# Kernel optimization log

Hardware: AMD Instinct MI355X
Metric: run time of the kernel (lower is better)

## Reference

```python
import jax, jax.numpy as jnp
import numpy as np

B, H, NQ, NL, NA = 262144, 256, 4, 2, 16


def _apply_1q(s, U, q):
    # s: [B, 2,2,2,2]; U: [B,2,2] (batched) or [2,2] (shared)
    s = jnp.moveaxis(s, 1 + q, -1)
    if U.ndim == 3:
        s = jnp.einsum('bij,b...j->b...i', U, s)
    else:
        s = jnp.einsum('ij,b...j->b...i', U, s)
    return jnp.moveaxis(s, -1, 1 + q)


def _apply_cnot(s, c, t):
    s = jnp.moveaxis(s, (1 + c, 1 + t), (-2, -1))
    s = jnp.stack([s[..., 0, :], s[..., 1, ::-1]], axis=-2)  # flip target when control=1
    return jnp.moveaxis(s, (-2, -1), (1 + c, 1 + t))


def _rx(theta):
    # batched RX: theta [B] -> [B,2,2]
    c = jnp.cos(theta / 2).astype(jnp.complex64)
    s = (-1j) * jnp.sin(theta / 2)
    return jnp.stack([jnp.stack([c, s], -1), jnp.stack([s, c], -1)], -2)


def _rot(phi, theta, omega):
    # PennyLane Rot = RZ(omega) @ RY(theta) @ RZ(phi), scalar angles -> [2,2]
    c, s = jnp.cos(theta / 2), jnp.sin(theta / 2)
    return jnp.array(1, jnp.complex64) * jnp.stack([
        jnp.stack([jnp.exp(-0.5j * (phi + omega)) * c, -jnp.exp(0.5j * (phi - omega)) * s], -1),
        jnp.stack([jnp.exp(-0.5j * (phi - omega)) * s, jnp.exp(0.5j * (phi + omega)) * c], -1),
    ], -2)


def _circuit(angles, q_weights):
    # angles: [B, NQ] -> PauliZ expvals [B, NQ] via 4-qubit state-vector sim
    b = angles.shape[0]
    s = jnp.zeros((b,) + (2,) * NQ, jnp.complex64)
    s = s.at[(slice(None),) + (0,) * NQ].set(1.0)
    for q in range(NQ):  # AngleEmbedding (RX rotations)
        s = _apply_1q(s, _rx(angles[:, q]), q)
    for l in range(NL):  # StronglyEntanglingLayers
        for w in range(NQ):
            s = _apply_1q(s, _rot(q_weights[l, w, 0], q_weights[l, w, 1], q_weights[l, w, 2]), w)
        r = l % (NQ - 1) + 1
        for w in range(NQ):
            s = _apply_cnot(s, w, (w + r) % NQ)
    probs = s.real ** 2 + s.imag ** 2  # [B,2,2,2,2]
    zs = []
    axes = tuple(range(1, NQ + 1))
    for q in range(NQ):
        p = probs.sum(tuple(a for a in axes if a != 1 + q))  # [B,2]
        zs.append(p[:, 0] - p[:, 1])
    return jnp.stack(zs, axis=1)


def setup_inputs() -> dict:
    key = jax.random.key(0)
    ks = jax.random.split(key, 6)
    return {
        'h': jax.random.normal(ks[0], (B, H), jnp.float32),
        'W_embed': jax.random.normal(ks[1], (NQ, H), jnp.float32) / np.sqrt(H),
        'b_embed': jnp.zeros((NQ,), jnp.float32),
        'q_weights': jax.random.uniform(ks[2], (NL, NQ, 3), jnp.float32, 0.0, 2 * np.pi),
        'W_out': jax.random.normal(ks[3], (NA, NQ), jnp.float32) / np.sqrt(NQ),
        'b_out': jnp.zeros((NA,), jnp.float32),
    }


def reference(h, W_embed, b_embed, q_weights, W_out, b_out):
    angles = jnp.tanh(h @ W_embed.T + b_embed)  # [B, NQ]
    z = _circuit(angles, q_weights)             # [B, NQ]
    return z @ W_out.T + b_out                  # [B, NA]
```

## Files before the change

kernel.cpp:

```cpp
#include <hip/hip_runtime.h>

#define NQ 4
#define NL 2
#define NA 16
#define HDIM 256
#define BLK 64
#define RPB 64

template<int M>
__device__ __forceinline__ void apply_u(float* sr, float* si, const float* u) {
    const float u00r = u[0], u00i = u[1], u01r = u[2], u01i = u[3];
    const float u10r = u[4], u10i = u[5], u11r = u[6], u11i = u[7];
#pragma unroll
    for (int k = 0; k < 16; ++k) {
        if (k & M) continue;
        const int k1 = k | M;
        const float a0r = sr[k],  a0i = si[k];
        const float a1r = sr[k1], a1i = si[k1];
        sr[k]  = u00r*a0r - u00i*a0i + u01r*a1r - u01i*a1i;
        si[k]  = u00r*a0i + u00i*a0r + u01r*a1i + u01i*a1r;
        sr[k1] = u10r*a0r - u10i*a0i + u11r*a1r - u11i*a1i;
        si[k1] = u10r*a0i + u10i*a0r + u11r*a1i + u11i*a1r;
    }
}

template<int MC, int MT>
__device__ __forceinline__ void cnot(float* sr, float* si) {
#pragma unroll
    for (int k = 0; k < 16; ++k) {
        if ((k & MC) && !(k & MT)) {
            const int k1 = k | MT;
            float tr = sr[k]; sr[k] = sr[k1]; sr[k1] = tr;
            float ti = si[k]; si[k] = si[k1]; si[k1] = ti;
        }
    }
}

__global__ __launch_bounds__(BLK) void qph_kernel(
    const float* __restrict__ h,
    const float* __restrict__ W_embed,
    const float* __restrict__ b_embed,
    const float* __restrict__ q_weights,
    const float* __restrict__ W_out,
    const float* __restrict__ b_out,
    float* __restrict__ out,
    int B)
{
    __shared__ __align__(16) float w_lds[NQ * HDIM];
    __shared__ float rot_lds[NL * NQ][8];
    __shared__ float wout_lds[NA * NQ];
    __shared__ float bout_lds[NA];

    const int tid = threadIdx.x;
    const long rowBase = (long)blockIdx.x * RPB;

#pragma unroll
    for (int k = 0; k < 16; ++k) w_lds[tid + k * BLK] = W_embed[tid + k * BLK];
    if (tid < NA * NQ) wout_lds[tid] = W_out[tid];
    if (tid < NA)      bout_lds[tid] = b_out[tid];
    if (tid < NL * NQ) {
        const float phi = q_weights[tid * 3 + 0];
        const float th  = q_weights[tid * 3 + 1];
        const float om  = q_weights[tid * 3 + 2];
        const float c  = cosf(0.5f * th), s  = sinf(0.5f * th);
        const float al = 0.5f * (phi + om), be = 0.5f * (phi - om);
        const float ca = cosf(al), sa = sinf(al);
        const float cb = cosf(be), sb = sinf(be);
        rot_lds[tid][0] =  ca * c;  rot_lds[tid][1] = -sa * c;
        rot_lds[tid][2] = -cb * s;  rot_lds[tid][3] = -sb * s;
        rot_lds[tid][4] =  cb * s;  rot_lds[tid][5] = -sb * s;
        rot_lds[tid][6] =  ca * c;  rot_lds[tid][7] =  sa * c;
    }
    __syncthreads();

    const int t = tid & 3;
    const int g = tid >> 2;
    const float be0 = b_embed[0], be1 = b_embed[1], be2 = b_embed[2], be3 = b_embed[3];

    float my0 = 0.f, my1 = 0.f, my2 = 0.f, my3 = 0.f;

#pragma unroll
    for (int rr = 0; rr < 4; ++rr) {
        const int  lrow = g * 4 + rr;
        const long grow = rowBase + lrow;
        float acc0 = 0.f, acc1 = 0.f, acc2 = 0.f, acc3 = 0.f;
        if (grow < B) {
            const float4* hrow = (const float4*)(h + grow * (long)HDIM);
#pragma unroll
            for (int j = 0; j < 16; ++j) {
                const float4 hv = hrow[j * 4 + t];
                const float4 w0 = *(const float4*)&w_lds[0 * HDIM + j * 16 + t * 4];
                const float4 w1 = *(const float4*)&w_lds[1 * HDIM + j * 16 + t * 4];
                const float4 w2 = *(const float4*)&w_lds[2 * HDIM + j * 16 + t * 4];
                const float4 w3 = *(const float4*)&w_lds[3 * HDIM + j * 16 + t * 4];
                acc0 = fmaf(hv.x, w0.x, fmaf(hv.y, w0.y, fmaf(hv.z, w0.z, fmaf(hv.w, w0.w, acc0))));
                acc1 = fmaf(hv.x, w1.x, fmaf(hv.y, w1.y, fmaf(hv.z, w1.z, fmaf(hv.w, w1.w, acc1))));
                acc2 = fmaf(hv.x, w2.x, fmaf(hv.y, w2.y, fmaf(hv.z, w2.z, fmaf(hv.w, w2.w, acc2))));
                acc3 = fmaf(hv.x, w3.x, fmaf(hv.y, w3.y, fmaf(hv.z, w3.z, fmaf(hv.w, w3.w, acc3))));
            }
        }
        acc0 += __shfl_xor(acc0, 1); acc0 += __shfl_xor(acc0, 2);
        acc1 += __shfl_xor(acc1, 1); acc1 += __shfl_xor(acc1, 2);
        acc2 += __shfl_xor(acc2, 1); acc2 += __shfl_xor(acc2, 2);
        acc3 += __shfl_xor(acc3, 1); acc3 += __shfl_xor(acc3, 2);
        if (t == rr) { my0 = acc0; my1 = acc1; my2 = acc2; my3 = acc3; }
    }

    const long grow = rowBase + tid;
    if (grow >= B) return;

    const float angs[4] = {tanhf(my0 + be0), tanhf(my1 + be1),
                           tanhf(my2 + be2), tanhf(my3 + be3)};

    float sr[16], si[16];
#pragma unroll
    for (int k = 0; k < 16; ++k) { sr[k] = 0.f; si[k] = 0.f; }
    sr[0] = 1.0f;

#pragma unroll
    for (int q = 0; q < NQ; ++q) {
        const float th = angs[q];
        const float c = __cosf(0.5f * th), s = __sinf(0.5f * th);
        const int m = 8 >> q;
#pragma unroll
        for (int k = 0; k < 16; ++k) {
            if (k & m) continue;
            const int k1 = k | m;
            const float a0r = sr[k],  a0i = si[k];
            const float a1r = sr[k1], a1i = si[k1];
            sr[k]  = c * a0r + s * a1i;
            si[k]  = c * a0i - s * a1r;
            sr[k1] = s * a0i + c * a1r;
            si[k1] = c * a1i - s * a0r;
        }
    }

    apply_u<8>(sr, si, rot_lds[0]);
    apply_u<4>(sr, si, rot_lds[1]);
    apply_u<2>(sr, si, rot_lds[2]);
    apply_u<1>(sr, si, rot_lds[3]);
    cnot<8, 4>(sr, si);
    cnot<4, 2>(sr, si);
    cnot<2, 1>(sr, si);
    cnot<1, 8>(sr, si);
    apply_u<8>(sr, si, rot_lds[4]);
    apply_u<4>(sr, si, rot_lds[5]);
    apply_u<2>(sr, si, rot_lds[6]);
    apply_u<1>(sr, si, rot_lds[7]);
    cnot<8, 2>(sr, si);
    cnot<4, 1>(sr, si);
    cnot<2, 8>(sr, si);
    cnot<1, 4>(sr, si);

    float p[16];
#pragma unroll
    for (int k = 0; k < 16; ++k) p[k] = sr[k] * sr[k] + si[k] * si[k];
    float z[4];
#pragma unroll
    for (int q = 0; q < NQ; ++q) {
        const int m = 8 >> q;
        float zz = 0.f;
#pragma unroll
        for (int k = 0; k < 16; ++k) zz += (k & m) ? -p[k] : p[k];
        z[q] = zz;
    }

    float4* out4 = (float4*)(out + grow * (long)NA);
#pragma unroll
    for (int i = 0; i < 4; ++i) {
        float o[4];
#pragma unroll
        for (int jj = 0; jj < 4; ++jj) {
            const int a = i * 4 + jj;
            float v = bout_lds[a];
#pragma unroll
            for (int q = 0; q < NQ; ++q) v = fmaf(z[q], wout_lds[a * 4 + q], v);
            o[jj] = v;
        }
        out4[i] = make_float4(o[0], o[1], o[2], o[3]);
    }
}

extern "C" void kernel_launch(void* const* d_in, const int* in_sizes, int n_in,
                              void* d_out, int out_size, void* d_ws, size_t ws_size,
                              hipStream_t stream) {
    const float* h         = (const float*)d_in[0];
    const float* W_embed   = (const float*)d_in[1];
    const float* b_embed   = (const float*)d_in[2];
    const float* q_weights = (const float*)d_in[3];
    const float* W_out     = (const float*)d_in[4];
    const float* b_out     = (const float*)d_in[5];
    float* out = (float*)d_out;

    const int B = in_sizes[0] / HDIM;
    const int blocks = (B + RPB - 1) / RPB;
    qph_kernel<<<blocks, BLK, 0, stream>>>(h, W_embed, b_embed, q_weights, W_out, b_out, out, B);
}
```

Before: 57.77 us.

## Double-buffer h rows into LDS via async global_load_lds with register-held weights

Raises the block to 256 threads and 256 rows, and streams h in 16-row tiles into a double-buffered LDS region using async global-to-LDS loads, overlapping the next tile's load with the current tile's dot products. W_embed now lives in registers per lane instead of LDS. The 16-lane shuffle reduction assigns each row's embedding to one thread, and z values are staged through LDS so each thread writes one output row. This adds register pressure and relies on hand-placed waitcnt values being correct. Each wave waits only on its own loads and there is no barrier between tiles, so reading rows loaded by other waves may be racy.

```diff
diff --git a/kernel.cpp b/kernel.cpp
--- a/kernel.cpp
+++ b/kernel.cpp
@@ -4,8 +4,16 @@
 #define NL 2
 #define NA 16
 #define HDIM 256
-#define BLK 64
-#define RPB 64
+#define BLK 256
+#define RPB 256
+#define TROWS 16
+#define NTILES (RPB / TROWS)
+
+__device__ __forceinline__ void gload_lds16(const float* g, float* l) {
+    __builtin_amdgcn_global_load_lds(
+        (const __attribute__((address_space(1))) void*)g,
+        (__attribute__((address_space(3))) void*)l, 16, 0, 0);
+}
 
 template<int M>
 __device__ __forceinline__ void apply_u(float* sr, float* si, const float* u) {
@@ -46,136 +54,164 @@
     float* __restrict__ out,
     int B)
 {
-    __shared__ __align__(16) float w_lds[NQ * HDIM];
+    __shared__ __align__(16) float hbuf[2][TROWS * HDIM];
     __shared__ float rot_lds[NL * NQ][8];
     __shared__ float wout_lds[NA * NQ];
     __shared__ float bout_lds[NA];
-
-    const int tid = threadIdx.x;
+    __shared__ __align__(16) float zbuf[RPB][4];
+
+    const int tid  = threadIdx.x;
+    const int lane = tid & 63;
+    const int w    = tid >> 6;
+    const int c    = lane & 15;
+    const int rit  = tid >> 4;
     const long rowBase = (long)blockIdx.x * RPB;
 
-#pragma unroll
-    for (int k = 0; k < 16; ++k) w_lds[tid + k * BLK] = W_embed[tid + k * BLK];
     if (tid < NA * NQ) wout_lds[tid] = W_out[tid];
     if (tid < NA)      bout_lds[tid] = b_out[tid];
     if (tid < NL * NQ) {
         const float phi = q_weights[tid * 3 + 0];
         const float th  = q_weights[tid * 3 + 1];
         const float om  = q_weights[tid * 3 + 2];
-        const float c  = cosf(0.5f * th), s  = sinf(0.5f * th);
+        const float cc = cosf(0.5f * th), ss = sinf(0.5f * th);
         const float al = 0.5f * (phi + om), be = 0.5f * (phi - om);
         const float ca = cosf(al), sa = sinf(al);
         const float cb = cosf(be), sb = sinf(be);
-        rot_lds[tid][0] =  ca * c;  rot_lds[tid][1] = -sa * c;
-        rot_lds[tid][2] = -cb * s;  rot_lds[tid][3] = -sb * s;
-        rot_lds[tid][4] =  cb * s;  rot_lds[tid][5] = -sb * s;
-        rot_lds[tid][6] =  ca * c;  rot_lds[tid][7] =  sa * c;
+        rot_lds[tid][0] =  ca * cc;  rot_lds[tid][1] = -sa * cc;
+        rot_lds[tid][2] = -cb * ss;  rot_lds[tid][3] = -sb * ss;
+        rot_lds[tid][4] =  cb * ss;  rot_lds[tid][5] = -sb * ss;
+        rot_lds[tid][6] =  ca * cc;  rot_lds[tid][7] =  sa * cc;
     }
     __syncthreads();
 
-    const int t = tid & 3;
-    const int g = tid >> 2;
+    float4 wreg[NQ][4];
+#pragma unroll
+    for (int q = 0; q < NQ; ++q)
+#pragma unroll
+        for (int j = 0; j < 4; ++j)
+            wreg[q][j] = *(const float4*)(W_embed + q * HDIM + c * 4 + j * 64);
     const float be0 = b_embed[0], be1 = b_embed[1], be2 = b_embed[2], be3 = b_embed[3];
 
+#define ISSUE_TILE(T, b)                                                        \
+    {                                                                           \
+        _Pragma("unroll")                                                       \
+        for (int r = 0; r < 4; ++r) {                                           \
+            long srow = rowBase + (long)(T) * TROWS + w * 4 + r;                \
+            if (srow > (long)B - 1) srow = (long)B - 1;                         \
+            gload_lds16(h + srow * HDIM + lane * 4,                             \
+                        &hbuf[b][(w * 4 + r) * HDIM]);                          \
+        }                                                                       \
+    }
+
+    ISSUE_TILE(0, 0);
+
     float my0 = 0.f, my1 = 0.f, my2 = 0.f, my3 = 0.f;
 
 #pragma unroll
-    for (int rr = 0; rr < 4; ++rr) {
-        const int  lrow = g * 4 + rr;
-        const long grow = rowBase + lrow;
-        float acc0 = 0.f, acc1 = 0.f, acc2 = 0.f, acc3 = 0.f;
-        if (grow < B) {
-            const float4* hrow = (const float4*)(h + grow * (long)HDIM);
-#pragma unroll
-            for (int j = 0; j < 16; ++j) {
-                const float4 hv = hrow[j * 4 + t];
-                const float4 w0 = *(const float4*)&w_lds[0 * HDIM + j * 16 + t * 4];
-                const float4 w1 = *(const float4*)&w_lds[1 * HDIM + j * 16 + t * 4];
-                const float4 w2 = *(const float4*)&w_lds[2 * HDIM + j * 16 + t * 4];
-                const float4 w3 = *(const float4*)&w_lds[3 * HDIM + j * 16 + t * 4];
-                acc0 = fmaf(hv.x, w0.x, fmaf(hv.y, w0.y, fmaf(hv.z, w0.z, fmaf(hv.w, w0.w, acc0))));
-                acc1 = fmaf(hv.x, w1.x, fmaf(hv.y, w1.y, fmaf(hv.z, w1.z, fmaf(hv.w, w1.w, acc1))));
-                acc2 = fmaf(hv.x, w2.x, fmaf(hv.y, w2.y, fmaf(hv.z, w2.z, fmaf(hv.w, w2.w, acc2))));
-                acc3 = fmaf(hv.x, w3.x, fmaf(hv.y, w3.y, fmaf(hv.z, w3.z, fmaf(hv.w, w3.w, acc3))));
+    for (int T = 0; T < NTILES; ++T) {
+        if (T + 1 < NTILES) {
+            ISSUE_TILE(T + 1, (T + 1) & 1);
+            asm volatile("s_waitcnt vmcnt(4)" ::: "memory");
+        } else {
+            asm volatile("s_waitcnt vmcnt(0)" ::: "memory");
+        }
+        __builtin_amdgcn_sched_barrier(0);
+
+        const float* hb = &hbuf[T & 1][rit * HDIM];
+        float a0 = 0.f, a1 = 0.f, a2 = 0.f, a3 = 0.f;
+#pragma unroll
+        for (int j = 0; j < 4; ++j) {
+            const float4 hv = *(const float4*)&hb[c * 4 + j * 64];
+            const float4 w0 = wreg[0][j], w1 = wreg[1][j], w2 = wreg[2][j], w3 = wreg[3][j];
+            a0 = fmaf(hv.x, w0.x, fmaf(hv.y, w0.y, fmaf(hv.z, w0.z, fmaf(hv.w, w0.w, a0))));
+            a1 = fmaf(hv.x, w1.x, fmaf(hv.y, w1.y, fmaf(hv.z, w1.z, fmaf(hv.w, w1.w, a1))));
+            a2 = fmaf(hv.x, w2.x, fmaf(hv.y, w2.y, fmaf(hv.z, w2.z, fmaf(hv.w, w2.w, a2))));
+            a3 = fmaf(hv.x, w3.x, fmaf(hv.y, w3.y, fmaf(hv.z, w3.z, fmaf(hv.w, w3.w, a3))));
+        }
+        a0 += __shfl_xor(a0, 1); a0 += __shfl_xor(a0, 2); a0 += __shfl_xor(a0, 4); a0 += __shfl_xor(a0, 8);
+        a1 += __shfl_xor(a1, 1); a1 += __shfl_xor(a1, 2); a1 += __shfl_xor(a1, 4); a1 += __shfl_xor(a1, 8);
+        a2 += __shfl_xor(a2, 1); a2 += __shfl_xor(a2, 2); a2 += __shfl_xor(a2, 4); a2 += __shfl_xor(a2, 8);
+        a3 += __shfl_xor(a3, 1); a3 += __shfl_xor(a3, 2); a3 += __shfl_xor(a3, 4); a3 += __shfl_xor(a3, 8);
+        if (c == T) { my0 = a0; my1 = a1; my2 = a2; my3 = a3; }
+    }
+#undef ISSUE_TILE
+
+    const int  lrow = c * 16 + rit;
+    const long grow = rowBase + lrow;
+
+    if (grow < B) {
+        const float angs[4] = {tanhf(my0 + be0), tanhf(my1 + be1),
+                               tanhf(my2 + be2), tanhf(my3 + be3)};
+
+        float sr[16], si[16];
+#pragma unroll
+        for (int k = 0; k < 16; ++k) { sr[k] = 0.f; si[k] = 0.f; }
+        sr[0] = 1.0f;
+
+#pragma unroll
+        for (int q = 0; q < NQ; ++q) {
+            const float th = angs[q];
+            const float cc = __cosf(0.5f * th), ss = __sinf(0.5f * th);
+            const int m = 8 >> q;
+#pragma unroll
+            for (int k = 0; k < 16; ++k) {
+                if (k & m) continue;
+                const int k1 = k | m;
+                const float r0 = sr[k],  i0 = si[k];
+                const float r1 = sr[k1], i1 = si[k1];
+                sr[k]  = cc * r0 + ss * i1;
+                si[k]  = cc * i0 - ss * r1;
+                sr[k1] = ss * i0 + cc * r1;
+                si[k1] = cc * i1 - ss * r0;
             }
         }
-        acc0 += __shfl_xor(acc0, 1); acc0 += __shfl_xor(acc0, 2);
-        acc1 += __shfl_xor(acc1, 1); acc1 += __shfl_xor(acc1, 2);
-        acc2 += __shfl_xor(acc2, 1); acc2 += __shfl_xor(acc2, 2);
-        acc3 += __shfl_xor(acc3, 1); acc3 += __shfl_xor(acc3, 2);
-        if (t == rr) { my0 = acc0; my1 = acc1; my2 = acc2; my3 = acc3; }
-    }
-
-    const long grow = rowBase + tid;
-    if (grow >= B) return;
-
-    const float angs[4] = {tanhf(my0 + be0), tanhf(my1 + be1),
-                           tanhf(my2 + be2), tanhf(my3 + be3)};
-
-    float sr[16], si[16];
-#pragma unroll
-    for (int k = 0; k < 16; ++k) { sr[k] = 0.f; si[k] = 0.f; }
-    sr[0] = 1.0f;
-
-#pragma unroll
-    for (int q = 0; q < NQ; ++q) {
-        const float th = angs[q];
-        const float c = __cosf(0.5f * th), s = __sinf(0.5f * th);
-        const int m = 8 >> q;
-#pragma unroll
-        for (int k = 0; k < 16; ++k) {
-            if (k & m) continue;
-            const int k1 = k | m;
-            const float a0r = sr[k],  a0i = si[k];
-            const float a1r = sr[k1], a1i = si[k1];
-            sr[k]  = c * a0r + s * a1i;
-            si[k]  = c * a0i - s * a1r;
-            sr[k1] = s * a0i + c * a1r;
-            si[k1] = c * a1i - s * a0r;
-        }
-    }
-
-    apply_u<8>(sr, si, rot_lds[0]);
-    apply_u<4>(sr, si, rot_lds[1]);
-    apply_u<2>(sr, si, rot_lds[2]);
-    apply_u<1>(sr, si, rot_lds[3]);
-    cnot<8, 4>(sr, si);
-    cnot<4, 2>(sr, si);
-    cnot<2, 1>(sr, si);
-    cnot<1, 8>(sr, si);
-    apply_u<8>(sr, si, rot_lds[4]);
-    apply_u<4>(sr, si, rot_lds[5]);
-    apply_u<2>(sr, si, rot_lds[6]);
-    apply_u<1>(sr, si, rot_lds[7]);
-    cnot<8, 2>(sr, si);
-    cnot<4, 1>(sr, si);
-    cnot<2, 8>(sr, si);
-    cnot<1, 4>(sr, si);
-
-    float p[16];
-#pragma unroll
-    for (int k = 0; k < 16; ++k) p[k] = sr[k] * sr[k] + si[k] * si[k];
-    float z[4];
-#pragma unroll
-    for (int q = 0; q < NQ; ++q) {
-        const int m = 8 >> q;
-        float zz = 0.f;
-#pragma unroll
-        for (int k = 0; k < 16; ++k) zz += (k & m) ? -p[k] : p[k];
-        z[q] = zz;
-    }
-
-    float4* out4 = (float4*)(out + grow * (long)NA);
+
+        apply_u<8>(sr, si, rot_lds[0]);
+        apply_u<4>(sr, si, rot_lds[1]);
+        apply_u<2>(sr, si, rot_lds[2]);
+        apply_u<1>(sr, si, rot_lds[3]);
+        cnot<8, 4>(sr, si);
+        cnot<4, 2>(sr, si);
+        cnot<2, 1>(sr, si);
+        cnot<1, 8>(sr, si);
+        apply_u<8>(sr, si, rot_lds[4]);
+        apply_u<4>(sr, si, rot_lds[5]);
+        apply_u<2>(sr, si, rot_lds[6]);
+        apply_u<1>(sr, si, rot_lds[7]);
+        cnot<8, 2>(sr, si);
+        cnot<4, 1>(sr, si);
+        cnot<2, 8>(sr, si);
+        cnot<1, 4>(sr, si);
+
+        float p[16];
+#pragma unroll
+        for (int k = 0; k < 16; ++k) p[k] = sr[k] * sr[k] + si[k] * si[k];
+        float zt[4];
+#pragma unroll
+        for (int q = 0; q < NQ; ++q) {
+            const int m = 8 >> q;
+            float zz = 0.f;
+#pragma unroll
+            for (int k = 0; k < 16; ++k) zz += (k & m) ? -p[k] : p[k];
+            zt[q] = zz;
+        }
+        *(float4*)&zbuf[lrow][0] = make_float4(zt[0], zt[1], zt[2], zt[3]);
+    }
+    __syncthreads();
+
+    const long orow = rowBase + tid;
+    if (orow >= B) return;
+    const float4 zv = *(const float4*)&zbuf[tid][0];
+
+    float4* out4 = (float4*)(out + orow * (long)NA);
 #pragma unroll
     for (int i = 0; i < 4; ++i) {
         float o[4];
 #pragma unroll
         for (int jj = 0; jj < 4; ++jj) {
             const int a = i * 4 + jj;
-            float v = bout_lds[a];
-#pragma unroll
-            for (int q = 0; q < NQ; ++q) v = fmaf(z[q], wout_lds[a * 4 + q], v);
-            o[jj] = v;
+            const float4 wv = *(const float4*)&wout_lds[a * 4];
+            o[jj] = bout_lds[a] + zv.x * wv.x + zv.y * wv.y + zv.z * wv.z + zv.w * wv.w;
         }
         out4[i] = make_float4(o[0], o[1], o[2], o[3]);
     }
```

New measurement: 62.42 us. +8.0%, slower.

## Stream h rows wave-wide with register-resident W_embed and butterfly reduction

Applied to the files above, without the earlier changes.

Restructures the embedding matvec so that each of the 64 lanes holds one float4 slice of every W_embed row in registers. The block then iterates over its 64 rows with fully coalesced 1 KB row loads, and the four per-row dot products are combined with a transposed shuffle butterfly. Results are redistributed to one row per thread through a small LDS buffer. This removes the LDS traffic for W_embed and gives contiguous global loads, at the cost of many more cross-lane shuffles per row and a fully unrolled 64-iteration loop.

```diff
diff --git a/kernel.cpp b/kernel.cpp
--- a/kernel.cpp
+++ b/kernel.cpp
@@ -6,6 +6,10 @@
 #define HDIM 256
 #define BLK 64
 #define RPB 64
+
+__device__ __forceinline__ float dot4(float4 a, float4 b) {
+    return fmaf(a.x, b.x, fmaf(a.y, b.y, fmaf(a.z, b.z, a.w * b.w)));
+}
 
 template<int M>
 __device__ __forceinline__ void apply_u(float* sr, float* si, const float* u) {
@@ -46,71 +50,84 @@
     float* __restrict__ out,
     int B)
 {
-    __shared__ __align__(16) float w_lds[NQ * HDIM];
     __shared__ float rot_lds[NL * NQ][8];
     __shared__ float wout_lds[NA * NQ];
     __shared__ float bout_lds[NA];
-
-    const int tid = threadIdx.x;
+    __shared__ __align__(16) float tbuf[RPB * 4];
+
+    const int l = threadIdx.x;
+    const int t = l & 3;
+    const int g = l >> 2;
     const long rowBase = (long)blockIdx.x * RPB;
 
-#pragma unroll
-    for (int k = 0; k < 16; ++k) w_lds[tid + k * BLK] = W_embed[tid + k * BLK];
-    if (tid < NA * NQ) wout_lds[tid] = W_out[tid];
-    if (tid < NA)      bout_lds[tid] = b_out[tid];
-    if (tid < NL * NQ) {
-        const float phi = q_weights[tid * 3 + 0];
-        const float th  = q_weights[tid * 3 + 1];
-        const float om  = q_weights[tid * 3 + 2];
+    if (l < NA * NQ) wout_lds[l] = W_out[l];
+    if (l < NA)      bout_lds[l] = b_out[l];
+    if (l < NL * NQ) {
+        const float phi = q_weights[l * 3 + 0];
+        const float th  = q_weights[l * 3 + 1];
+        const float om  = q_weights[l * 3 + 2];
         const float c  = cosf(0.5f * th), s  = sinf(0.5f * th);
         const float al = 0.5f * (phi + om), be = 0.5f * (phi - om);
         const float ca = cosf(al), sa = sinf(al);
         const float cb = cosf(be), sb = sinf(be);
-        rot_lds[tid][0] =  ca * c;  rot_lds[tid][1] = -sa * c;
-        rot_lds[tid][2] = -cb * s;  rot_lds[tid][3] = -sb * s;
-        rot_lds[tid][4] =  cb * s;  rot_lds[tid][5] = -sb * s;
-        rot_lds[tid][6] =  ca * c;  rot_lds[tid][7] =  sa * c;
-    }
+        rot_lds[l][0] =  ca * c;  rot_lds[l][1] = -sa * c;
+        rot_lds[l][2] = -cb * s;  rot_lds[l][3] = -sb * s;
+        rot_lds[l][4] =  cb * s;  rot_lds[l][5] = -sb * s;
+        rot_lds[l][6] =  ca * c;  rot_lds[l][7] =  sa * c;
+    }
+
+    float4 wq0 = *(const float4*)(W_embed + 0 * HDIM + 4 * l);
+    float4 wq1 = *(const float4*)(W_embed + 1 * HDIM + 4 * l);
+    float4 wq2 = *(const float4*)(W_embed + 2 * HDIM + 4 * l);
+    float4 wq3 = *(const float4*)(W_embed + 3 * HDIM + 4 * l);
     __syncthreads();
 
-    const int t = tid & 3;
-    const int g = tid >> 2;
-    const float be0 = b_embed[0], be1 = b_embed[1], be2 = b_embed[2], be3 = b_embed[3];
-
-    float my0 = 0.f, my1 = 0.f, my2 = 0.f, my3 = 0.f;
-
-#pragma unroll
-    for (int rr = 0; rr < 4; ++rr) {
-        const int  lrow = g * 4 + rr;
-        const long grow = rowBase + lrow;
-        float acc0 = 0.f, acc1 = 0.f, acc2 = 0.f, acc3 = 0.f;
-        if (grow < B) {
-            const float4* hrow = (const float4*)(h + grow * (long)HDIM);
-#pragma unroll
-            for (int j = 0; j < 16; ++j) {
-                const float4 hv = hrow[j * 4 + t];
-                const float4 w0 = *(const float4*)&w_lds[0 * HDIM + j * 16 + t * 4];
-                const float4 w1 = *(const float4*)&w_lds[1 * HDIM + j * 16 + t * 4];
-                const float4 w2 = *(const float4*)&w_lds[2 * HDIM + j * 16 + t * 4];
-                const float4 w3 = *(const float4*)&w_lds[3 * HDIM + j * 16 + t * 4];
-                acc0 = fmaf(hv.x, w0.x, fmaf(hv.y, w0.y, fmaf(hv.z, w0.z, fmaf(hv.w, w0.w, acc0))));
-                acc1 = fmaf(hv.x, w1.x, fmaf(hv.y, w1.y, fmaf(hv.z, w1.z, fmaf(hv.w, w1.w, acc1))));
-                acc2 = fmaf(hv.x, w2.x, fmaf(hv.y, w2.y, fmaf(hv.z, w2.z, fmaf(hv.w, w2.w, acc2))));
-                acc3 = fmaf(hv.x, w3.x, fmaf(hv.y, w3.y, fmaf(hv.z, w3.z, fmaf(hv.w, w3.w, acc3))));
-            }
-        }
-        acc0 += __shfl_xor(acc0, 1); acc0 += __shfl_xor(acc0, 2);
-        acc1 += __shfl_xor(acc1, 1); acc1 += __shfl_xor(acc1, 2);
-        acc2 += __shfl_xor(acc2, 1); acc2 += __shfl_xor(acc2, 2);
-        acc3 += __shfl_xor(acc3, 1); acc3 += __shfl_xor(acc3, 2);
-        if (t == rr) { my0 = acc0; my1 = acc1; my2 = acc2; my3 = acc3; }
-    }
-
-    const long grow = rowBase + tid;
+    float keep0 = 0.f, keep1 = 0.f, keep2 = 0.f, keep3 = 0.f;
+    const float4* __restrict__ h4 = (const float4*)h;
+
+#pragma unroll
+    for (int it = 0; it < RPB; ++it) {
+        long ro = rowBase + it; if (ro >= B) ro = B - 1;
+        const float4 hv = h4[ro * 64 + l];
+
+        const float p0 = dot4(hv, wq0);
+        const float p1 = dot4(hv, wq1);
+        const float p2 = dot4(hv, wq2);
+        const float p3 = dot4(hv, wq3);
+
+        float a01 = (l & 1) ? p1 : p0;
+        float b01 = (l & 1) ? p0 : p1;
+        a01 += __shfl_xor(b01, 1);
+        float a23 = (l & 1) ? p3 : p2;
+        float b23 = (l & 1) ? p2 : p3;
+        a23 += __shfl_xor(b23, 1);
+        float aa = (l & 2) ? a23 : a01;
+        float bb = (l & 2) ? a01 : a23;
+        aa += __shfl_xor(bb, 2);
+        aa += __shfl_xor(aa, 4);
+        aa += __shfl_xor(aa, 8);
+        aa += __shfl_xor(aa, 16);
+        aa += __shfl_xor(aa, 32);
+        if ((it >> 2) == g) {
+            if ((it & 3) == 0) keep0 = aa;
+            if ((it & 3) == 1) keep1 = aa;
+            if ((it & 3) == 2) keep2 = aa;
+            if ((it & 3) == 3) keep3 = aa;
+        }
+    }
+
+    tbuf[(g * 4 + 0) * 4 + t] = keep0;
+    tbuf[(g * 4 + 1) * 4 + t] = keep1;
+    tbuf[(g * 4 + 2) * 4 + t] = keep2;
+    tbuf[(g * 4 + 3) * 4 + t] = keep3;
+    __syncthreads();
+    const float4 sv = *(const float4*)&tbuf[l * 4];
+
+    const long grow = rowBase + l;
     if (grow >= B) return;
 
-    const float angs[4] = {tanhf(my0 + be0), tanhf(my1 + be1),
-                           tanhf(my2 + be2), tanhf(my3 + be3)};
+    const float angs[4] = {tanhf(sv.x + b_embed[0]), tanhf(sv.y + b_embed[1]),
+                           tanhf(sv.z + b_embed[2]), tanhf(sv.w + b_embed[3])};
 
     float sr[16], si[16];
 #pragma unroll
```

Result: slower. 61.75 us (+6.9%).
